# Performance work log

Measured on AMD Instinct MI355X. Metric: run time of the kernel, lower is better.

Reference implementation:

```python
import jax, jax.numpy as jnp
import numpy as np

NUM_GROUPS = 2048  # ix values drawn from [0, NUM_GROUPS); stands in for torch.unique's group count

def setup_inputs() -> dict:
    key = jax.random.key(0)
    ks = jax.random.split(key, 9)
    B, E, D = 2, 32768, 512
    s = 1.0 / np.sqrt(D)  # nn.Linear default init scale
    x = jax.random.normal(ks[0], (B, E, D), jnp.float32)
    ix = jax.random.randint(ks[1], (E,), 0, NUM_GROUPS)
    Wf = jax.random.uniform(ks[2], (D, D), jnp.float32, -s, s)
    bf = jax.random.uniform(ks[3], (D,), jnp.float32, -s, s)
    Wg = jax.random.uniform(ks[4], (D, D), jnp.float32, -s, s)
    bg = jax.random.uniform(ks[5], (D,), jnp.float32, -s, s)
    Wh = jax.random.uniform(ks[6], (D, D), jnp.float32, -s, s)
    bh = jax.random.uniform(ks[7], (D,), jnp.float32, -s, s)
    return {"x": x, "ix": ix, "Wf": Wf, "bf": bf, "Wg": Wg, "bg": bg, "Wh": Wh, "bh": bh}

def reference(x, ix, Wf, bf, Wg, bg, Wh, bh):
    # Linear projections (nn.Linear: x @ W.T + b)
    logits = jnp.einsum('bed,kd->bek', x, Wg) + bg  # g(x): (B,E,D)
    vals   = jnp.einsum('bed,kd->bek', x, Wf) + bf  # f(x): (B,E,D)
    # Move edges to leading axis for segment ops: (E,B,D)
    lt = jnp.transpose(logits, (1, 0, 2))
    vt = jnp.transpose(vals, (1, 0, 2))
    # Group-wise (scatter) softmax over edges sharing the same ix
    m = jax.ops.segment_max(lt, ix, num_segments=NUM_GROUPS)      # (G,B,D)
    e = jnp.exp(lt - m[ix])                                        # (E,B,D)
    denom = jax.ops.segment_sum(e, ix, num_segments=NUM_GROUPS)   # (G,B,D)
    w = e / denom[ix]                                              # (E,B,D)
    # Weighted scatter-sum per group
    y = jax.ops.segment_sum(vt * w, ix, num_segments=NUM_GROUPS)  # (G,B,D)
    y = jnp.transpose(y, (1, 0, 2))                                # (B,G,D)
    out = jnp.einsum('bgd,kd->bgk', y, Wh) + bh                    # h(y)
    return out[:, ix]                                              # expand back to (B,E,D)
```

## Files before the change

### kernel.cpp

```cpp
#include <hip/hip_runtime.h>
#include <hip/hip_bf16.h>
#include <cstdint>
#include <cstddef>

typedef __bf16 bf16x8 __attribute__((ext_vector_type(8)));
typedef float f32x4 __attribute__((ext_vector_type(4)));
using u16 = unsigned short;

#define NUM_GROUPS_C 2048

__device__ __forceinline__ u16 f2bf(float f) {
  union { float f; uint32_t u; } c; c.f = f;
  uint32_t r = (c.u + 0x7fffu + ((c.u >> 16) & 1u)) >> 16;
  return (u16)r;
}
__device__ __forceinline__ float bf2f(u16 h) {
  union { uint32_t u; float f; } c; c.u = ((uint32_t)h) << 16; return c.f;
}

__device__ __forceinline__ void glds16(const u16* g, void* l) {
  __builtin_amdgcn_global_load_lds((const __attribute__((address_space(1))) void*)g,
                                   (__attribute__((address_space(3))) void*)l, 16, 0, 0);
}

__global__ void cast_f32_bf16(const float* __restrict__ src, u16* __restrict__ dst, long n4) {
  long i = (long)blockIdx.x * blockDim.x + threadIdx.x;
  long stride = (long)gridDim.x * blockDim.x;
  for (; i < n4; i += stride) {
    float4 v = reinterpret_cast<const float4*>(src)[i];
    uint2 o;
    o.x = (uint32_t)f2bf(v.x) | ((uint32_t)f2bf(v.y) << 16);
    o.y = (uint32_t)f2bf(v.z) | ((uint32_t)f2bf(v.w) << 16);
    reinterpret_cast<uint2*>(dst)[i] = o;
  }
}

__global__ void zero_i32(int* p, int n) {
  int i = blockIdx.x * blockDim.x + threadIdx.x;
  if (i < n) p[i] = 0;
}
__global__ void count_k(const int* __restrict__ ix, int* __restrict__ cnt, int E) {
  int e = blockIdx.x * blockDim.x + threadIdx.x;
  if (e < E) atomicAdd(&cnt[ix[e]], 1);
}
__global__ void scan_k(const int* __restrict__ cnt, int* __restrict__ offs,
                       int* __restrict__ cursor, int G) {
  __shared__ int part[256];
  int t = threadIdx.x;
  int gpt = G / 256;
  int base = t * gpt;
  int loc[8];
  int s = 0;
  for (int j = 0; j < gpt; ++j) { loc[j] = cnt[base + j]; s += loc[j]; }
  part[t] = s;
  __syncthreads();
  for (int off = 1; off < 256; off <<= 1) {
    int v = (t >= off) ? part[t - off] : 0;
    __syncthreads();
    part[t] += v;
    __syncthreads();
  }
  int run = part[t] - s;
  for (int j = 0; j < gpt; ++j) {
    offs[base + j] = run;
    cursor[base + j] = run;
    run += loc[j];
  }
}
__global__ void scatter_k(const int* __restrict__ ix, int* __restrict__ cursor,
                          int* __restrict__ elist, int E) {
  int e = blockIdx.x * blockDim.x + threadIdx.x;
  if (e < E) {
    int g = ix[e];
    int pos = atomicAdd(&cursor[g], 1);
    elist[pos] = e;
  }
}

__global__ __launch_bounds__(512, 2)
void gemm256_bf16_nt(const u16* __restrict__ A,
                     const u16* __restrict__ B0, const u16* __restrict__ B1,
                     const float* __restrict__ bias0, const float* __restrict__ bias1,
                     u16* __restrict__ C0, u16* __restrict__ C1,
                     int K, int N) {
  __shared__ u16 lds[2 * 32768];

  const int tid  = threadIdx.x;
  const int lane = tid & 63;
  const int wid  = tid >> 6;
  const int wm   = wid >> 2;
  const int wn   = wid & 3;
  const int fr   = lane & 15;
  const int fq   = lane >> 4;
  const int swr  = fr & 7;

  const int nwg = gridDim.x;
  const int cpx = nwg >> 3;
  const int wg  = blockIdx.x;
  const int swz = (wg & 7) * cpx + (wg >> 3);
  const int mt = swz >> 2;
  const int ns = swz & 3;
  const u16* Bm  = (ns < 2) ? B0 : B1;
  const float* bias = (ns < 2) ? bias0 : bias1;
  u16* C = (ns < 2) ? C0 : C1;
  const int n0 = (ns & 1) * 256;
  const int m0 = mt * 256;

  const int r8   = tid >> 3;
  const int scol = ((tid & 7) ^ (r8 & 7)) << 3;
  const u16* Ab = A  + (size_t)m0 * K + scol;
  const u16* Bb = Bm + (size_t)n0 * K + scol;

  auto stage = [&](int buf, int k0) {
    u16* bufA = lds + buf * 32768;
    u16* bufB = bufA + 16384;
    #pragma unroll
    for (int i = 0; i < 4; ++i)
      glds16(Ab + (size_t)(i * 64 + r8) * K + k0, (char*)bufA + i * 8192 + wid * 1024);
    #pragma unroll
    for (int i = 0; i < 4; ++i)
      glds16(Bb + (size_t)(i * 64 + r8) * K + k0, (char*)bufB + i * 8192 + wid * 1024);
  };

  f32x4 acc[8][4] = {};
  const int NT = K >> 6;

  stage(0, 0);

  for (int t = 0; t < NT; ++t) {
    const int c = t & 1;
    if (t + 1 < NT) {
      stage(c ^ 1, (t + 1) << 6);
      asm volatile("s_waitcnt vmcnt(8)" ::: "memory");
    } else {
      asm volatile("s_waitcnt vmcnt(0)" ::: "memory");
    }
    __builtin_amdgcn_s_barrier();

    const char* sA_ = (const char*)(lds + c * 32768);
    const char* sB_ = sA_ + 32768;

    #pragma unroll
    for (int q = 0; q < 4; ++q) {
      const int qm = q >> 1, qn = q & 1;
      bf16x8 av[4][2], bv[2][2];
      #pragma unroll
      for (int j = 0; j < 4; ++j)
        #pragma unroll
        for (int kk = 0; kk < 2; ++kk)
          av[j][kk] = *(const bf16x8*)(sA_ + ((wm * 128 + (qm * 4 + j) * 16 + fr) << 7)
                                           + ((((kk << 2) | fq) ^ swr) << 4));
      #pragma unroll
      for (int j = 0; j < 2; ++j)
        #pragma unroll
        for (int kk = 0; kk < 2; ++kk)
          bv[j][kk] = *(const bf16x8*)(sB_ + ((wn * 64 + (qn * 2 + j) * 16 + fr) << 7)
                                           + ((((kk << 2) | fq) ^ swr) << 4));
      __builtin_amdgcn_s_barrier();
      __builtin_amdgcn_s_setprio(1);
      #pragma unroll
      for (int j = 0; j < 4; ++j)
        #pragma unroll
        for (int jn = 0; jn < 2; ++jn)
          #pragma unroll
          for (int kk = 0; kk < 2; ++kk)
            acc[qm * 4 + j][qn * 2 + jn] = __builtin_amdgcn_mfma_f32_16x16x32_bf16(
                av[j][kk], bv[jn][kk], acc[qm * 4 + j][qn * 2 + jn], 0, 0, 0);
      __builtin_amdgcn_s_setprio(0);
      __builtin_amdgcn_s_barrier();
      __builtin_amdgcn_sched_barrier(0);
    }
  }

  #pragma unroll
  for (int mi = 0; mi < 8; ++mi) {
    const int row = m0 + wm * 128 + mi * 16 + fq * 4;
    #pragma unroll
    for (int ni = 0; ni < 4; ++ni) {
      const int col = n0 + wn * 64 + ni * 16 + fr;
      const float bvv = bias[col];
      #pragma unroll
      for (int r = 0; r < 4; ++r)
        C[(size_t)(row + r) * N + col] = f2bf(acc[mi][ni][r] + bvv);
    }
  }
}

__device__ __forceinline__ void stage_tile_128x64(const u16* __restrict__ src, int ld,
                                                  u16* lds, int tid) {
  int wid = tid >> 6;
  #pragma unroll
  for (int i = 0; i < 4; ++i) {
    int c = i * 256 + tid;
    const u16* g = src + (size_t)(c >> 3) * ld + ((c & 7) << 3);
    char* l = (char*)lds + ((i * 4 + wid) << 10);
    glds16(g, l);
  }
}

__global__ __launch_bounds__(256)
void gemm_bf16_nt_f32out(const u16* __restrict__ A, const u16* __restrict__ Bm,
                         const float* __restrict__ bias,
                         float* __restrict__ C, int K, int N) {
  __shared__ u16 sA[128 * 64];
  __shared__ u16 sB[128 * 64];

  int tid = threadIdx.x;
  const int m0 = blockIdx.x * 128, n0 = blockIdx.y * 128;
  const u16* Ap = A + (size_t)m0 * K;
  const u16* Bp = Bm + (size_t)n0 * K;

  int lane = tid & 63;
  int wid = tid >> 6;
  int wm = wid >> 1, wn = wid & 1;
  int fr = lane & 15;
  int fq = lane >> 4;

  f32x4 acc[4][4] = {};

  for (int k0 = 0; k0 < K; k0 += 64) {
    stage_tile_128x64(Ap + k0, K, sA, tid);
    stage_tile_128x64(Bp + k0, K, sB, tid);
    __syncthreads();
    #pragma unroll
    for (int kk = 0; kk < 2; ++kk) {
      bf16x8 af[4], bfrag[4];
      #pragma unroll
      for (int mi = 0; mi < 4; ++mi)
        af[mi] = *reinterpret_cast<const bf16x8*>(&sA[(wm * 64 + mi * 16 + fr) * 64 + kk * 32 + fq * 8]);
      #pragma unroll
      for (int nj = 0; nj < 4; ++nj)
        bfrag[nj] = *reinterpret_cast<const bf16x8*>(&sB[(wn * 64 + nj * 16 + fr) * 64 + kk * 32 + fq * 8]);
      #pragma unroll
      for (int mi = 0; mi < 4; ++mi)
        #pragma unroll
        for (int nj = 0; nj < 4; ++nj)
          acc[mi][nj] = __builtin_amdgcn_mfma_f32_16x16x32_bf16(af[mi], bfrag[nj], acc[mi][nj], 0, 0, 0);
    }
    __syncthreads();
  }

  #pragma unroll
  for (int nj = 0; nj < 4; ++nj) {
    int col = n0 + wn * 64 + nj * 16 + fr;
    float bv = bias[col];
    #pragma unroll
    for (int mi = 0; mi < 4; ++mi) {
      int rowb = m0 + wm * 64 + mi * 16 + fq * 4;
      #pragma unroll
      for (int r = 0; r < 4; ++r)
        C[(size_t)(rowb + r) * N + col] = acc[mi][nj][r] + bv;
    }
  }
}

__global__ __launch_bounds__(256)
void seg_softmax(const u16* __restrict__ lg, const u16* __restrict__ vl,
                 const int* __restrict__ cnt, const int* __restrict__ offs,
                 const int* __restrict__ elist,
                 u16* __restrict__ y, int E, int D, int B, int G) {
  __shared__ int eids[256];
  int g = blockIdx.x / B;
  int b = blockIdx.x - g * B;
  int t = threadIdx.x;
  int n = cnt[g], start = offs[g];
  int d0 = t * 2;

  float m0 = -1e30f, m1 = -1e30f, s0 = 0.f, s1 = 0.f, a0 = 0.f, a1 = 0.f;
  for (int c0 = 0; c0 < n; c0 += 256) {
    int nc = n - c0; if (nc > 256) nc = 256;
    __syncthreads();
    if (t < nc) eids[t] = elist[start + c0 + t];
    __syncthreads();
    for (int i = 0; i < nc; ++i) {
      size_t base = ((size_t)b * E + eids[i]) * D + d0;
      uint32_t lu = *reinterpret_cast<const uint32_t*>(lg + base);
      uint32_t vu = *reinterpret_cast<const uint32_t*>(vl + base);
      float l0 = bf2f((u16)(lu & 0xffffu)), l1 = bf2f((u16)(lu >> 16));
      float v0 = bf2f((u16)(vu & 0xffffu)), v1 = bf2f((u16)(vu >> 16));
      float nm0 = fmaxf(m0, l0);
      float sc0 = __expf(m0 - nm0), w0 = __expf(l0 - nm0);
      s0 = s0 * sc0 + w0; a0 = a0 * sc0 + w0 * v0; m0 = nm0;
      float nm1 = fmaxf(m1, l1);
      float sc1 = __expf(m1 - nm1), w1 = __expf(l1 - nm1);
      s1 = s1 * sc1 + w1; a1 = a1 * sc1 + w1 * v1; m1 = nm1;
    }
  }
  float r0 = (n > 0) ? a0 / s0 : 0.f;
  float r1 = (n > 0) ? a1 / s1 : 0.f;
  size_t yoff = ((size_t)b * G + g) * D + d0;
  uint32_t o = (uint32_t)f2bf(r0) | ((uint32_t)f2bf(r1) << 16);
  *reinterpret_cast<uint32_t*>(y + yoff) = o;
}

__global__ void gather_k(const float* __restrict__ of, const int* __restrict__ ix,
                         float* __restrict__ out, int E, int D, int G) {
  int be = blockIdx.x;
  int b = be / E;
  int e = be - b * E;
  int gsel = ix[e];
  const float4* src = reinterpret_cast<const float4*>(of + ((size_t)b * G + gsel) * D);
  float4* dst = reinterpret_cast<float4*>(out + (size_t)be * D);
  for (int t = threadIdx.x; t < D / 4; t += blockDim.x)
    dst[t] = src[t];
}

extern "C" void kernel_launch(void* const* d_in, const int* in_sizes, int n_in,
                              void* d_out, int out_size, void* d_ws, size_t ws_size,
                              hipStream_t stream) {
  const float* x   = (const float*)d_in[0];
  const int*   ix  = (const int*)d_in[1];
  const float* Wf  = (const float*)d_in[2];
  const float* bfb = (const float*)d_in[3];
  const float* Wg  = (const float*)d_in[4];
  const float* bg  = (const float*)d_in[5];
  const float* Wh  = (const float*)d_in[6];
  const float* bh  = (const float*)d_in[7];

  const int E = in_sizes[1];
  const int D = in_sizes[3];
  const int B = in_sizes[0] / (E * D);
  const int G = NUM_GROUPS_C;
  const int M = B * E;
  const long xn = (long)M * D;

  char* ws = (char*)d_ws;
  size_t off = 0;
  auto alloc = [&](size_t bytes) -> char* {
    char* p = ws + off;
    off += (bytes + 255) & ~(size_t)255;
    return p;
  };
  u16* xb  = (u16*)alloc((size_t)M * D * 2);
  u16* lgb = (u16*)alloc((size_t)M * D * 2);
  u16* vlb = (u16*)alloc((size_t)M * D * 2);
  u16* Wgb = (u16*)alloc((size_t)D * D * 2);
  u16* Wfb = (u16*)alloc((size_t)D * D * 2);
  u16* Whb = (u16*)alloc((size_t)D * D * 2);
  u16* yb  = (u16*)alloc((size_t)B * G * D * 2);
  float* ofb = (float*)alloc((size_t)B * G * D * 4);
  int* cnt    = (int*)alloc((size_t)G * 4);
  int* offs   = (int*)alloc((size_t)G * 4);
  int* cursor = (int*)alloc((size_t)G * 4);
  int* elist  = (int*)alloc((size_t)E * 4);

  cast_f32_bf16<<<2048, 256, 0, stream>>>(x, xb, xn / 4);
  cast_f32_bf16<<<64, 256, 0, stream>>>(Wg, Wgb, (long)D * D / 4);
  cast_f32_bf16<<<64, 256, 0, stream>>>(Wf, Wfb, (long)D * D / 4);
  cast_f32_bf16<<<64, 256, 0, stream>>>(Wh, Whb, (long)D * D / 4);

  zero_i32<<<(G + 255) / 256, 256, 0, stream>>>(cnt, G);
  count_k<<<(E + 255) / 256, 256, 0, stream>>>(ix, cnt, E);
  scan_k<<<1, 256, 0, stream>>>(cnt, offs, cursor, G);
  scatter_k<<<(E + 255) / 256, 256, 0, stream>>>(ix, cursor, elist, E);

  gemm256_bf16_nt<<<(M / 256) * 4, 512, 0, stream>>>(xb, Wgb, Wfb, bg, bfb, lgb, vlb, D, D);

  seg_softmax<<<G * B, 256, 0, stream>>>(lgb, vlb, cnt, offs, elist, yb, E, D, B, G);

  dim3 gh((B * G) / 128, D / 128);
  gemm_bf16_nt_f32out<<<gh, 256, 0, stream>>>(yb, Whb, bh, ofb, D, D);

  gather_k<<<B * E, 128, 0, stream>>>(ofb, ix, (float*)d_out, E, D, G);
}
```

Baseline: 242.2 us.

## Fuse fp32-to-bf16 cast of x into projection GEMM A-tile loading

Removes the separate cast kernel that converted x to a bf16 workspace copy. The GEMM now loads fp32 A rows into registers, converts them to bf16 and writes them to swizzled LDS, while B still streams through global_load_lds. The three weight casts are merged into one launch. This cuts a full read and write pass over x, but doubles the global bytes the GEMM reads for A, adds register pressure, and drops the intra-loop barriers and setprio scheduling.

```diff
diff --git a/kernel.cpp b/kernel.cpp
--- a/kernel.cpp
+++ b/kernel.cpp
@@ -23,9 +23,14 @@
                                    (__attribute__((address_space(3))) void*)l, 16, 0, 0);
 }
 
-__global__ void cast_f32_bf16(const float* __restrict__ src, u16* __restrict__ dst, long n4) {
-  long i = (long)blockIdx.x * blockDim.x + threadIdx.x;
-  long stride = (long)gridDim.x * blockDim.x;
+__global__ void cast_w3(const float* __restrict__ w0, const float* __restrict__ w1,
+                        const float* __restrict__ w2,
+                        u16* __restrict__ o0, u16* __restrict__ o1, u16* __restrict__ o2,
+                        int n4) {
+  const float* src = (blockIdx.y == 0) ? w0 : (blockIdx.y == 1) ? w1 : w2;
+  u16* dst = (blockIdx.y == 0) ? o0 : (blockIdx.y == 1) ? o1 : o2;
+  int i = blockIdx.x * blockDim.x + threadIdx.x;
+  int stride = gridDim.x * blockDim.x;
   for (; i < n4; i += stride) {
     float4 v = reinterpret_cast<const float4*>(src)[i];
     uint2 o;
@@ -78,11 +83,11 @@
 }
 
 __global__ __launch_bounds__(512, 2)
-void gemm256_bf16_nt(const u16* __restrict__ A,
-                     const u16* __restrict__ B0, const u16* __restrict__ B1,
-                     const float* __restrict__ bias0, const float* __restrict__ bias1,
-                     u16* __restrict__ C0, u16* __restrict__ C1,
-                     int K, int N) {
+void gemm256_fg(const float* __restrict__ A,
+                const u16* __restrict__ B0, const u16* __restrict__ B1,
+                const float* __restrict__ bias0, const float* __restrict__ bias1,
+                u16* __restrict__ C0, u16* __restrict__ C1,
+                int K, int N) {
   __shared__ u16 lds[2 * 32768];
 
   const int tid  = threadIdx.x;
@@ -100,40 +105,64 @@
   const int swz = (wg & 7) * cpx + (wg >> 3);
   const int mt = swz >> 2;
   const int ns = swz & 3;
-  const u16* Bm  = (ns < 2) ? B0 : B1;
+  const u16* Bm     = (ns < 2) ? B0 : B1;
   const float* bias = (ns < 2) ? bias0 : bias1;
-  u16* C = (ns < 2) ? C0 : C1;
+  u16* C            = (ns < 2) ? C0 : C1;
   const int n0 = (ns & 1) * 256;
   const int m0 = mt * 256;
 
+  const int ar = tid >> 1;
+  const int ah = tid & 1;
+  const float* Asrc = A + (size_t)(m0 + ar) * K + ah * 32;
+
   const int r8   = tid >> 3;
   const int scol = ((tid & 7) ^ (r8 & 7)) << 3;
-  const u16* Ab = A  + (size_t)m0 * K + scol;
   const u16* Bb = Bm + (size_t)n0 * K + scol;
 
-  auto stage = [&](int buf, int k0) {
-    u16* bufA = lds + buf * 32768;
-    u16* bufB = bufA + 16384;
-    #pragma unroll
-    for (int i = 0; i < 4; ++i)
-      glds16(Ab + (size_t)(i * 64 + r8) * K + k0, (char*)bufA + i * 8192 + wid * 1024);
+  f32x4 aregs[8];
+  auto loadA = [&](int k0) {
+    #pragma unroll
+    for (int k = 0; k < 8; ++k)
+      aregs[k] = *reinterpret_cast<const f32x4*>(Asrc + k0 + k * 4);
+  };
+  auto stageB = [&](int buf, int k0) {
+    u16* bufB = lds + buf * 32768 + 16384;
     #pragma unroll
     for (int i = 0; i < 4; ++i)
       glds16(Bb + (size_t)(i * 64 + r8) * K + k0, (char*)bufB + i * 8192 + wid * 1024);
   };
+  auto writeA = [&](int buf) {
+    u16* bufA = lds + buf * 32768;
+    #pragma unroll
+    for (int k = 0; k < 4; ++k) {
+      bf16x8 w;
+      #pragma unroll
+      for (int j = 0; j < 4; ++j) {
+        w[j]     = (__bf16)aregs[2 * k][j];
+        w[4 + j] = (__bf16)aregs[2 * k + 1][j];
+      }
+      const int slot = (ah * 4 + k) ^ (ar & 7);
+      *reinterpret_cast<bf16x8*>(&bufA[(size_t)ar * 64 + slot * 8]) = w;
+    }
+  };
 
   f32x4 acc[8][4] = {};
   const int NT = K >> 6;
 
-  stage(0, 0);
+  loadA(0);
+  stageB(0, 0);
 
   for (int t = 0; t < NT; ++t) {
     const int c = t & 1;
+    __builtin_amdgcn_s_barrier();
+    asm volatile("s_waitcnt vmcnt(4)" ::: "memory");
+    writeA(c);
     if (t + 1 < NT) {
-      stage(c ^ 1, (t + 1) << 6);
-      asm volatile("s_waitcnt vmcnt(8)" ::: "memory");
+      loadA((t + 1) << 6);
+      stageB(c ^ 1, (t + 1) << 6);
+      asm volatile("s_waitcnt vmcnt(12) lgkmcnt(0)" ::: "memory");
     } else {
-      asm volatile("s_waitcnt vmcnt(0)" ::: "memory");
+      asm volatile("s_waitcnt vmcnt(0) lgkmcnt(0)" ::: "memory");
     }
     __builtin_amdgcn_s_barrier();
 
@@ -156,8 +185,6 @@
         for (int kk = 0; kk < 2; ++kk)
           bv[j][kk] = *(const bf16x8*)(sB_ + ((wn * 64 + (qn * 2 + j) * 16 + fr) << 7)
                                            + ((((kk << 2) | fq) ^ swr) << 4));
-      __builtin_amdgcn_s_barrier();
-      __builtin_amdgcn_s_setprio(1);
       #pragma unroll
       for (int j = 0; j < 4; ++j)
         #pragma unroll
@@ -166,9 +193,6 @@
           for (int kk = 0; kk < 2; ++kk)
             acc[qm * 4 + j][qn * 2 + jn] = __builtin_amdgcn_mfma_f32_16x16x32_bf16(
                 av[j][kk], bv[jn][kk], acc[qm * 4 + j][qn * 2 + jn], 0, 0, 0);
-      __builtin_amdgcn_s_setprio(0);
-      __builtin_amdgcn_s_barrier();
-      __builtin_amdgcn_sched_barrier(0);
     }
   }
 
@@ -322,7 +346,6 @@
   const int B = in_sizes[0] / (E * D);
   const int G = NUM_GROUPS_C;
   const int M = B * E;
-  const long xn = (long)M * D;
 
   char* ws = (char*)d_ws;
   size_t off = 0;
@@ -331,7 +354,6 @@
     off += (bytes + 255) & ~(size_t)255;
     return p;
   };
-  u16* xb  = (u16*)alloc((size_t)M * D * 2);
   u16* lgb = (u16*)alloc((size_t)M * D * 2);
   u16* vlb = (u16*)alloc((size_t)M * D * 2);
   u16* Wgb = (u16*)alloc((size_t)D * D * 2);
@@ -344,17 +366,15 @@
   int* cursor = (int*)alloc((size_t)G * 4);
   int* elist  = (int*)alloc((size_t)E * 4);
 
-  cast_f32_bf16<<<2048, 256, 0, stream>>>(x, xb, xn / 4);
-  cast_f32_bf16<<<64, 256, 0, stream>>>(Wg, Wgb, (long)D * D / 4);
-  cast_f32_bf16<<<64, 256, 0, stream>>>(Wf, Wfb, (long)D * D / 4);
-  cast_f32_bf16<<<64, 256, 0, stream>>>(Wh, Whb, (long)D * D / 4);
+  dim3 gw(64, 3);
+  cast_w3<<<gw, 256, 0, stream>>>(Wg, Wf, Wh, Wgb, Wfb, Whb, D * D / 4);
 
   zero_i32<<<(G + 255) / 256, 256, 0, stream>>>(cnt, G);
   count_k<<<(E + 255) / 256, 256, 0, stream>>>(ix, cnt, E);
   scan_k<<<1, 256, 0, stream>>>(cnt, offs, cursor, G);
   scatter_k<<<(E + 255) / 256, 256, 0, stream>>>(ix, cursor, elist, E);
 
-  gemm256_bf16_nt<<<(M / 256) * 4, 512, 0, stream>>>(xb, Wgb, Wfb, bg, bfb, lgb, vlb, D, D);
+  gemm256_fg<<<(M / 256) * 4, 512, 0, stream>>>(x, Wgb, Wfb, bg, bfb, lgb, vlb, D, D);
 
   seg_softmax<<<G * B, 256, 0, stream>>>(lgb, vlb, cnt, offs, elist, yb, E, D, B, G);
 
```

Result: faster. 237.3 us (-2.1%).

## Rework projection GEMM into 4-phase interleaved load/MFMA pipeline; fuse weight casts

Applied to the files above, without the earlier changes.

Restructures the 256x256 bf16 projection GEMM so that each K-step is split into four quadrant phases. Each phase issues one half-tile global-to-LDS load for the next buffer while the MFMAs for the current quadrant run, with finer vmcnt waits and barriers. The warp-to-fragment mapping is interleaved (rows mi*32+wm*16, cols ni*64+wn*16) to match the half-tile staging. The three weight cast launches are merged into one 2D-grid kernel to cut launch overhead. This adds more barriers per K-step and relies on correct vmcnt accounting; the last iteration re-stages a redundant tile.

```diff
diff --git a/kernel.cpp b/kernel.cpp
--- a/kernel.cpp
+++ b/kernel.cpp
@@ -26,6 +26,23 @@
 __global__ void cast_f32_bf16(const float* __restrict__ src, u16* __restrict__ dst, long n4) {
   long i = (long)blockIdx.x * blockDim.x + threadIdx.x;
   long stride = (long)gridDim.x * blockDim.x;
+  for (; i < n4; i += stride) {
+    float4 v = reinterpret_cast<const float4*>(src)[i];
+    uint2 o;
+    o.x = (uint32_t)f2bf(v.x) | ((uint32_t)f2bf(v.y) << 16);
+    o.y = (uint32_t)f2bf(v.z) | ((uint32_t)f2bf(v.w) << 16);
+    reinterpret_cast<uint2*>(dst)[i] = o;
+  }
+}
+
+__global__ void cast_w3(const float* __restrict__ w0, const float* __restrict__ w1,
+                        const float* __restrict__ w2,
+                        u16* __restrict__ o0, u16* __restrict__ o1, u16* __restrict__ o2,
+                        int n4) {
+  const float* src = (blockIdx.y == 0) ? w0 : (blockIdx.y == 1) ? w1 : w2;
+  u16* dst = (blockIdx.y == 0) ? o0 : (blockIdx.y == 1) ? o1 : o2;
+  int i = blockIdx.x * blockDim.x + threadIdx.x;
+  int stride = gridDim.x * blockDim.x;
   for (; i < n4; i += stride) {
     float4 v = reinterpret_cast<const float4*>(src)[i];
     uint2 o;
@@ -78,12 +95,12 @@
 }
 
 __global__ __launch_bounds__(512, 2)
-void gemm256_bf16_nt(const u16* __restrict__ A,
-                     const u16* __restrict__ B0, const u16* __restrict__ B1,
-                     const float* __restrict__ bias0, const float* __restrict__ bias1,
-                     u16* __restrict__ C0, u16* __restrict__ C1,
-                     int K, int N) {
-  __shared__ u16 lds[2 * 32768];
+void gemm256_fg8(const u16* __restrict__ A,
+                 const u16* __restrict__ B0g, const u16* __restrict__ B1g,
+                 const float* __restrict__ bias0, const float* __restrict__ bias1,
+                 u16* __restrict__ C0, u16* __restrict__ C1,
+                 int K, int N) {
+  __shared__ u16 lds[65536];
 
   const int tid  = threadIdx.x;
   const int lane = tid & 63;
@@ -94,96 +111,106 @@
   const int fq   = lane >> 4;
   const int swr  = fr & 7;
 
-  const int nwg = gridDim.x;
-  const int cpx = nwg >> 3;
-  const int wg  = blockIdx.x;
+  const int nwg = gridDim.x, cpx = nwg >> 3, wg = blockIdx.x;
   const int swz = (wg & 7) * cpx + (wg >> 3);
-  const int mt = swz >> 2;
-  const int ns = swz & 3;
-  const u16* Bm  = (ns < 2) ? B0 : B1;
+  const int mt = swz >> 2, ns = swz & 3;
+  const u16* Bm     = (ns < 2) ? B0g : B1g;
   const float* bias = (ns < 2) ? bias0 : bias1;
-  u16* C = (ns < 2) ? C0 : C1;
-  const int n0 = (ns & 1) * 256;
-  const int m0 = mt * 256;
+  u16* C            = (ns < 2) ? C0 : C1;
+  const int n0 = (ns & 1) * 256, m0 = mt * 256;
 
   const int r8   = tid >> 3;
   const int scol = ((tid & 7) ^ (r8 & 7)) << 3;
   const u16* Ab = A  + (size_t)m0 * K + scol;
   const u16* Bb = Bm + (size_t)n0 * K + scol;
-
-  auto stage = [&](int buf, int k0) {
-    u16* bufA = lds + buf * 32768;
-    u16* bufB = bufA + 16384;
-    #pragma unroll
-    for (int i = 0; i < 4; ++i)
-      glds16(Ab + (size_t)(i * 64 + r8) * K + k0, (char*)bufA + i * 8192 + wid * 1024);
-    #pragma unroll
-    for (int i = 0; i < 4; ++i)
-      glds16(Bb + (size_t)(i * 64 + r8) * K + k0, (char*)bufB + i * 8192 + wid * 1024);
+  char* ldsb = (char*)lds;
+
+  auto stage_ht = [&](int p, int isB, int h, int kt) {
+    const u16* src = (isB ? Bb : Ab) + (size_t)(h * 128 + r8) * K + kt * 64;
+    char* dst = ldsb + p * 65536 + isB * 32768 + h * 16384 + wid * 1024;
+    glds16(src, dst);
+    glds16(src + (size_t)64 * K, dst + 8192);
   };
+
+#define RD_A(dst, mi_, kk_) \
+  dst = *(const bf16x8*)(sA_ + (((mi_) * 32 + wm * 16 + fr) << 7) + (((((kk_) << 2) | fq) ^ swr) << 4))
+#define RD_B(dst, nj_, kk_) \
+  dst = *(const bf16x8*)(sB_ + (((nj_) * 64 + wn * 16 + fr) << 7) + (((((kk_) << 2) | fq) ^ swr) << 4))
+#define MFMA_Q(accm, accn, af, bf_)                                                \
+  __builtin_amdgcn_s_setprio(1);                                                  \
+  _Pragma("unroll") for (int j = 0; j < 4; ++j)                                    \
+  _Pragma("unroll") for (int jn = 0; jn < 2; ++jn)                                 \
+  _Pragma("unroll") for (int kk = 0; kk < 2; ++kk)                                 \
+    acc[(accm) + j][(accn) + jn] = __builtin_amdgcn_mfma_f32_16x16x32_bf16(        \
+        af[j][kk], bf_[jn][kk], acc[(accm) + j][(accn) + jn], 0, 0, 0);            \
+  __builtin_amdgcn_s_setprio(0);
 
   f32x4 acc[8][4] = {};
   const int NT = K >> 6;
 
-  stage(0, 0);
-
-  for (int t = 0; t < NT; ++t) {
-    const int c = t & 1;
-    if (t + 1 < NT) {
-      stage(c ^ 1, (t + 1) << 6);
-      asm volatile("s_waitcnt vmcnt(8)" ::: "memory");
-    } else {
-      asm volatile("s_waitcnt vmcnt(0)" ::: "memory");
-    }
-    __builtin_amdgcn_s_barrier();
-
-    const char* sA_ = (const char*)(lds + c * 32768);
+  stage_ht(0, 1, 0, 0);
+  stage_ht(0, 0, 0, 0);
+  stage_ht(0, 1, 1, 0);
+  stage_ht(0, 0, 1, 0);
+  asm volatile("s_waitcnt vmcnt(4)" ::: "memory");
+  __builtin_amdgcn_s_barrier();
+
+  for (int kt = 0; kt < NT; ++kt) {
+    const int cb = kt & 1, nb = cb ^ 1;
+    const int ks = (kt + 1 < NT) ? kt + 1 : NT - 1;
+    const char* sA_ = ldsb + cb * 65536;
     const char* sB_ = sA_ + 32768;
-
-    #pragma unroll
-    for (int q = 0; q < 4; ++q) {
-      const int qm = q >> 1, qn = q & 1;
-      bf16x8 av[4][2], bv[2][2];
-      #pragma unroll
-      for (int j = 0; j < 4; ++j)
-        #pragma unroll
-        for (int kk = 0; kk < 2; ++kk)
-          av[j][kk] = *(const bf16x8*)(sA_ + ((wm * 128 + (qm * 4 + j) * 16 + fr) << 7)
-                                           + ((((kk << 2) | fq) ^ swr) << 4));
-      #pragma unroll
-      for (int j = 0; j < 2; ++j)
-        #pragma unroll
-        for (int kk = 0; kk < 2; ++kk)
-          bv[j][kk] = *(const bf16x8*)(sB_ + ((wn * 64 + (qn * 2 + j) * 16 + fr) << 7)
-                                           + ((((kk << 2) | fq) ^ swr) << 4));
-      __builtin_amdgcn_s_barrier();
-      __builtin_amdgcn_s_setprio(1);
-      #pragma unroll
-      for (int j = 0; j < 4; ++j)
-        #pragma unroll
-        for (int jn = 0; jn < 2; ++jn)
-          #pragma unroll
-          for (int kk = 0; kk < 2; ++kk)
-            acc[qm * 4 + j][qn * 2 + jn] = __builtin_amdgcn_mfma_f32_16x16x32_bf16(
-                av[j][kk], bv[jn][kk], acc[qm * 4 + j][qn * 2 + jn], 0, 0, 0);
-      __builtin_amdgcn_s_setprio(0);
-      __builtin_amdgcn_s_barrier();
-      __builtin_amdgcn_sched_barrier(0);
-    }
-  }
+    bf16x8 a0[4][2], a1[4][2], b0[2][2], b1[2][2];
+
+    #pragma unroll
+    for (int j = 0; j < 4; ++j) { RD_A(a0[j][0], j, 0); RD_A(a0[j][1], j, 1); }
+    #pragma unroll
+    for (int j = 0; j < 2; ++j) { RD_B(b0[j][0], j, 0); RD_B(b0[j][1], j, 1); }
+    stage_ht(nb, 1, 0, ks);
+    asm volatile("s_waitcnt vmcnt(4)" ::: "memory");
+    __builtin_amdgcn_s_barrier();
+    MFMA_Q(0, 0, a0, b0)
+    __builtin_amdgcn_s_barrier();
+
+    #pragma unroll
+    for (int j = 0; j < 2; ++j) { RD_B(b1[j][0], j + 2, 0); RD_B(b1[j][1], j + 2, 1); }
+    stage_ht(nb, 0, 0, ks);
+    asm volatile("s_waitcnt vmcnt(4)" ::: "memory");
+    __builtin_amdgcn_s_barrier();
+    MFMA_Q(0, 2, a0, b1)
+    __builtin_amdgcn_s_barrier();
+
+    #pragma unroll
+    for (int j = 0; j < 4; ++j) { RD_A(a1[j][0], j + 4, 0); RD_A(a1[j][1], j + 4, 1); }
+    stage_ht(nb, 1, 1, ks);
+    asm volatile("s_waitcnt vmcnt(4)" ::: "memory");
+    __builtin_amdgcn_s_barrier();
+    MFMA_Q(4, 2, a1, b1)
+    __builtin_amdgcn_s_barrier();
+
+    stage_ht(nb, 0, 1, ks);
+    asm volatile("s_waitcnt vmcnt(4)" ::: "memory");
+    __builtin_amdgcn_s_barrier();
+    MFMA_Q(4, 0, a1, b0)
+    __builtin_amdgcn_s_barrier();
+  }
+  asm volatile("s_waitcnt vmcnt(0)" ::: "memory");
 
   #pragma unroll
   for (int mi = 0; mi < 8; ++mi) {
-    const int row = m0 + wm * 128 + mi * 16 + fq * 4;
+    const int row = m0 + mi * 32 + wm * 16 + fq * 4;
     #pragma unroll
     for (int ni = 0; ni < 4; ++ni) {
-      const int col = n0 + wn * 64 + ni * 16 + fr;
+      const int col = n0 + ni * 64 + wn * 16 + fr;
       const float bvv = bias[col];
       #pragma unroll
       for (int r = 0; r < 4; ++r)
         C[(size_t)(row + r) * N + col] = f2bf(acc[mi][ni][r] + bvv);
     }
   }
+#undef RD_A
+#undef RD_B
+#undef MFMA_Q
 }
 
 __device__ __forceinline__ void stage_tile_128x64(const u16* __restrict__ src, int ld,
@@ -345,16 +372,15 @@
   int* elist  = (int*)alloc((size_t)E * 4);
 
   cast_f32_bf16<<<2048, 256, 0, stream>>>(x, xb, xn / 4);
-  cast_f32_bf16<<<64, 256, 0, stream>>>(Wg, Wgb, (long)D * D / 4);
-  cast_f32_bf16<<<64, 256, 0, stream>>>(Wf, Wfb, (long)D * D / 4);
-  cast_f32_bf16<<<64, 256, 0, stream>>>(Wh, Whb, (long)D * D / 4);
+  dim3 gw(64, 3);
+  cast_w3<<<gw, 256, 0, stream>>>(Wg, Wf, Wh, Wgb, Wfb, Whb, D * D / 4);
 
   zero_i32<<<(G + 255) / 256, 256, 0, stream>>>(cnt, G);
   count_k<<<(E + 255) / 256, 256, 0, stream>>>(ix, cnt, E);
   scan_k<<<1, 256, 0, stream>>>(cnt, offs, cursor, G);
   scatter_k<<<(E + 255) / 256, 256, 0, stream>>>(ix, cursor, elist, E);
 
-  gemm256_bf16_nt<<<(M / 256) * 4, 512, 0, stream>>>(xb, Wgb, Wfb, bg, bfb, lgb, vlb, D, D);
+  gemm256_fg8<<<(M / 256) * 4, 512, 0, stream>>>(xb, Wgb, Wfb, bg, bfb, lgb, vlb, D, D);
 
   seg_softmax<<<G * B, 256, 0, stream>>>(lgb, vlb, cnt, offs, elist, yb, E, D, B, G);
 
```

Result: faster. 222.0 us (-8.4%).
